# Kernel tuning notes

Hardware: AMD Instinct MI355X
Metric: run time of the kernel (lower is better)

Reference implementation:

```python
import jax, jax.numpy as jnp
import numpy as np

B, T, C, H = 4, 2048, 1024, 16
D = C // H  # head dim = 64
ROPE_BASE = 10000.0


def _rope_cache(seq_len, dim, dtype=jnp.float32):
    # torchtune-style interleaved RoPE cache
    inv_freq = 1.0 / (ROPE_BASE ** (jnp.arange(0, dim, 2, dtype=jnp.float32) / dim))
    t = jnp.arange(seq_len, dtype=jnp.float32)
    freqs = jnp.outer(t, inv_freq)  # [T, D/2]
    return jnp.cos(freqs).astype(dtype), jnp.sin(freqs).astype(dtype)


def _apply_rope(x, cos, sin):
    # x: [B, H, T, D]; rotate interleaved pairs along last dim
    x1 = x[..., 0::2]
    x2 = x[..., 1::2]
    # broadcast cos/sin [T, D/2] -> [1, 1, T, D/2]
    o1 = x1 * cos - x2 * sin
    o2 = x2 * cos + x1 * sin
    out = jnp.stack([o1, o2], axis=-1).reshape(x.shape)
    return out


def setup_inputs() -> dict:
    key = jax.random.key(0)
    k1, k2, k3 = jax.random.split(key, 3)
    x = jax.random.normal(k1, (B, T, C), dtype=jnp.float32)
    W_in = jax.random.normal(k2, (C, 3 * C), dtype=jnp.float32) * (1.0 / np.sqrt(C))
    b_in = jnp.zeros((3 * C,), dtype=jnp.float32)
    W_out = jax.random.normal(k3, (C, C), dtype=jnp.float32) * (1.0 / np.sqrt(C))
    b_out = jnp.zeros((C,), dtype=jnp.float32)
    return {"x": x, "W_in": W_in, "b_in": b_in, "W_out": W_out, "b_out": b_out}


def reference(x, W_in, b_in, W_out, b_out):
    Bx, Tx, Cx = x.shape
    qkv = x @ W_in + b_in                      # [B, T, 3C]
    q, k, v = jnp.split(qkv, 3, axis=-1)
    # [B, T, C] -> [B, H, T, D]
    def to_heads(t):
        return t.reshape(Bx, Tx, H, D).transpose(0, 2, 1, 3)
    q, k, v = to_heads(q), to_heads(k), to_heads(v)

    cos, sin = _rope_cache(Tx, D, dtype=x.dtype)
    q = _apply_rope(q, cos, sin)
    k = _apply_rope(k, cos, sin)

    scale = 1.0 / np.sqrt(D)
    att = jnp.einsum('bhqd,bhkd->bhqk', q, k) * scale   # [B, H, T, T]
    causal = jnp.tril(jnp.ones((Tx, Tx), dtype=bool))
    att = jnp.where(causal[None, None, :, :], att, jnp.float32(-jnp.inf).astype(att.dtype))
    att = jax.nn.softmax(att, axis=-1)
    # dropout = 0.0 (eval mode): identity
    y = jnp.einsum('bhqk,bhkd->bhqd', att, v)           # [B, H, T, D]
    y = y.transpose(0, 2, 1, 3).reshape(Bx, Tx, Cx)     # [B, T, C]
    return y @ W_out + b_out
```

## Files before the change

### kernel.cpp

```cpp
#include <hip/hip_runtime.h>

#define B_ 4
#define T_ 2048
#define C_ 1024
#define H_ 16
#define D_ 64
#define M_ (B_*T_)
#define N3_ (3*C_)
#define NQT_ 16

typedef unsigned short u16;
typedef short bf16x8 __attribute__((ext_vector_type(8)));
typedef short bf16x4 __attribute__((ext_vector_type(4)));
typedef unsigned short u16x8 __attribute__((ext_vector_type(8)));
typedef unsigned int u32x4 __attribute__((ext_vector_type(4)));
typedef float f32x4 __attribute__((ext_vector_type(4)));
typedef float f32x16 __attribute__((ext_vector_type(16)));

#define QSCALE 0.18033688f
#define DEFER_THR 11.0f

__device__ __forceinline__ u16 f2bf(float f) {
  unsigned u = __float_as_uint(f);
  u += 0x7fffu + ((u >> 16) & 1u);
  return (u16)(u >> 16);
}

__device__ __forceinline__ unsigned cvt_pk_bf16(float lo, float hi) {
  unsigned r;
  asm("v_cvt_pk_bf16_f32 %0, %1, %2" : "=v"(r) : "v"(lo), "v"(hi));
  return r;
}

__device__ __forceinline__ void gload16(const void* g, void* l) {
  __builtin_amdgcn_global_load_lds((const __attribute__((address_space(1))) void*)g,
                                   (__attribute__((address_space(3))) void*)l, 16, 0, 0);
}

__device__ __forceinline__ int epi_key(int ml) { return (ml ^ (ml >> 3)) & 7; }

__global__ __launch_bounds__(256) void k_prep(const float* __restrict__ x,
                                              u16* __restrict__ xbf,
                                              const float* __restrict__ W_in,
                                              u16* __restrict__ WtIn,
                                              const float* __restrict__ W_out,
                                              u16* __restrict__ WtOut,
                                              float* __restrict__ ct,
                                              float* __restrict__ st) {
  __shared__ float tile[64][65];
  const int bx = blockIdx.x, tid = threadIdx.x;
  if (bx < 4096) {
    int i = bx * 256 + tid;
    f32x4 a = *(const f32x4*)(x + (size_t)i * 8);
    f32x4 b = *(const f32x4*)(x + (size_t)i * 8 + 4);
    u16x8 o;
    #pragma unroll
    for (int j = 0; j < 4; ++j) { o[j] = f2bf(a[j]); o[4 + j] = f2bf(b[j]); }
    *(u16x8*)(xbf + (size_t)i * 8) = o;
  } else if (bx < 5120) {
    const float* W; u16* Wt; int K = C_, N, b;
    if (bx < 4864) { W = W_in; Wt = WtIn; N = N3_; b = bx - 4096; }
    else           { W = W_out; Wt = WtOut; N = C_; b = bx - 4864; }
    int ntiles = N / 64;
    int n0 = (b % ntiles) * 64, k0 = (b / ntiles) * 64;
    int c = tid & 63, r0 = tid >> 6;
    #pragma unroll
    for (int i = 0; i < 16; ++i) {
      int r = i * 4 + r0;
      tile[r][c] = W[(size_t)(k0 + r) * N + n0 + c];
    }
    __syncthreads();
    #pragma unroll
    for (int i = 0; i < 16; ++i) {
      int r = i * 4 + r0;
      Wt[(size_t)(n0 + r) * K + k0 + c] = f2bf(tile[c][r]);
    }
  } else {
    int idx = (bx - 5120) * 256 + tid;
    int t = idx >> 5, i = idx & 31;
    double inv = exp(-(2.0 * (double)i / 64.0) * log(10000.0));
    double a = (double)t * inv;
    ct[idx] = (float)cos(a);
    st[idx] = (float)sin(a);
  }
}

__global__ __launch_bounds__(512) void k_gemm1(const u16* __restrict__ A,
                                               const u16* __restrict__ Bt,
                                               const float* __restrict__ bias,
                                               u16* __restrict__ Qb, u16* __restrict__ Kb,
                                               u16* __restrict__ Vt,
                                               const float* __restrict__ ctab,
                                               const float* __restrict__ stab) {
  __shared__ u16 lds[128 * 64 + 256 * 64];
  u16* sA = lds;
  u16* sB = lds + 128 * 64;
  const int tid = threadIdx.x, lane = tid & 63, w = tid >> 6;
  const int g = lane >> 4, r = lane & 15;
  const int wm = w >> 2, wn = w & 3;
  const int Kd = C_;
  const int lin = blockIdx.y * gridDim.x + blockIdx.x;
  const int tM = ((lin & 7) * 8 + ((lin >> 3) & 7)) * 128;
  const int tN = (lin >> 6) * 256;

  f32x4 acc[4][4];
  #pragma unroll
  for (int i = 0; i < 4; ++i)
    #pragma unroll
    for (int j = 0; j < 4; ++j) acc[i][j] = (f32x4){0.f, 0.f, 0.f, 0.f};

  for (int k0 = 0; k0 < Kd; k0 += 64) {
    #pragma unroll
    for (int i = 0; i < 2; ++i) {
      int c = i * 512 + tid, row = c >> 3, slot = (c & 7) ^ (row & 7);
      gload16(A + (size_t)(tM + row) * Kd + k0 + slot * 8, sA + (i * 512 + w * 64) * 8);
    }
    #pragma unroll
    for (int i = 0; i < 4; ++i) {
      int c = i * 512 + tid, row = c >> 3, slot = (c & 7) ^ (row & 7);
      gload16(Bt + (size_t)(tN + row) * Kd + k0 + slot * 8, sB + (i * 512 + w * 64) * 8);
    }
    __syncthreads();
    bf16x8 af[4][2], bfr[4][2];
    #pragma unroll
    for (int mt = 0; mt < 4; ++mt)
      #pragma unroll
      for (int kk = 0; kk < 2; ++kk) {
        int row = wm * 64 + mt * 16 + r;
        af[mt][kk] = *(const bf16x8*)(sA + ((row * 64 + kk * 32 + g * 8) ^ ((row & 7) << 3)));
      }
    #pragma unroll
    for (int nt = 0; nt < 4; ++nt)
      #pragma unroll
      for (int kk = 0; kk < 2; ++kk) {
        int row = wn * 64 + nt * 16 + r;
        bfr[nt][kk] = *(const bf16x8*)(sB + ((row * 64 + kk * 32 + g * 8) ^ ((row & 7) << 3)));
      }
    __builtin_amdgcn_s_setprio(1);
    #pragma unroll
    for (int mt = 0; mt < 4; ++mt)
      #pragma unroll
      for (int nt = 0; nt < 4; ++nt)
        #pragma unroll
        for (int kk = 0; kk < 2; ++kk)
          acc[mt][nt] = __builtin_amdgcn_mfma_f32_16x16x32_bf16(af[mt][kk], bfr[nt][kk],
                                                                acc[mt][nt], 0, 0, 0);
    __builtin_amdgcn_s_setprio(0);
    __syncthreads();
  }

  const int secb = tN >> 10;
  u16* tile = lds;
  const int bb = tM >> 11;
  #pragma unroll
  for (int hN = 0; hN < 2; ++hN) {
    if ((wn >> 1) == hN) {
      #pragma unroll
      for (int mt = 0; mt < 4; ++mt)
        #pragma unroll
        for (int nt = 0; nt < 4; ++nt) {
          int nl = (wn & 1) * 64 + nt * 16 + r;
          int n = tN + hN * 128 + nl;
          float bv = bias[n];
          int dd = n & 63;
          #pragma unroll
          for (int reg = 0; reg < 4; ++reg) {
            int ml = wm * 64 + mt * 16 + g * 4 + reg;
            int tt = (tM + ml) & (T_ - 1);
            float v = acc[mt][nt][reg] + bv;
            if (secb < 2) {
              float pv = __shfl_xor(v, 1);
              int pi = tt * 32 + (dd >> 1);
              float c = ctab[pi], sn = stab[pi];
              v = (dd & 1) ? (v * c + pv * sn) : (v * c - pv * sn);
              if (secb == 0) v *= QSCALE;
            }
            tile[ml * 128 + ((((nl >> 3) ^ epi_key(ml)) << 3) | (nl & 7))] = f2bf(v);
          }
        }
    }
    __syncthreads();
    if (secb < 2) {
      u16* dst = secb == 0 ? Qb : Kb;
      #pragma unroll
      for (int i = 0; i < 4; ++i) {
        int idx = i * 512 + tid;
        int row = idx >> 4, cc = idx & 15;
        u16x8 val = *(const u16x8*)(tile + row * 128 + ((cc ^ epi_key(row)) << 3));
        int n = tN + hN * 128 + cc * 8;
        int m = tM + row;
        int hh = (n & 1023) >> 6, dd = n & 63;
        int tt = m & (T_ - 1);
        *(u16x8*)(dst + ((size_t)(bb * H_ + hh) * T_ + tt) * D_ + dd) = val;
      }
    } else {
      const int tt0 = tM & (T_ - 1);
      #pragma unroll
      for (int i = 0; i < 4; ++i) {
        int idx = i * 512 + tid;
        int nl = idx >> 4, tg = idx & 15;
        u16x8 val;
        #pragma unroll
        for (int j = 0; j < 8; ++j) {
          int ml = tg * 8 + j;
          val[j] = tile[ml * 128 + ((((nl >> 3) ^ epi_key(ml)) << 3) | (nl & 7))];
        }
        int n = tN + hN * 128 + nl;
        int hh = (n & 1023) >> 6, dd = n & 63;
        *(u16x8*)(Vt + ((size_t)(bb * H_ + hh) * D_ + dd) * T_ + tt0 + tg * 8) = val;
      }
    }
    __syncthreads();
  }
}

__global__ __launch_bounds__(256) void k_gemm2(const u16* __restrict__ A,
                                               const u16* __restrict__ Bt,
                                               const float* __restrict__ bias,
                                               float* __restrict__ Cout,
                                               int Nd, int Kd) {
  __shared__ u16 sA[128 * 128];
  __shared__ u16 sB[128 * 128];
  const int tid = threadIdx.x, lane = tid & 63, w = tid >> 6;
  const int g = lane >> 4, r = lane & 15;
  const int wm = w >> 1, wn = w & 1;
  const int lin = blockIdx.y * gridDim.x + blockIdx.x;
  const int tM = ((lin & 7) * 8 + ((lin >> 3) & 7)) * 128;
  const int tN = (lin >> 6) * 128;

  f32x4 acc[4][4];
  #pragma unroll
  for (int i = 0; i < 4; ++i)
    #pragma unroll
    for (int j = 0; j < 4; ++j) acc[i][j] = (f32x4){0.f, 0.f, 0.f, 0.f};

  for (int k0 = 0; k0 < Kd; k0 += 128) {
    #pragma unroll
    for (int i = 0; i < 8; ++i) {
      int c = i * 256 + tid, row = c >> 4, slot = (c & 15) ^ (row & 15);
      gload16(A + (size_t)(tM + row) * Kd + k0 + slot * 8, sA + (i * 256 + w * 64) * 8);
    }
    #pragma unroll
    for (int i = 0; i < 8; ++i) {
      int c = i * 256 + tid, row = c >> 4, slot = (c & 15) ^ (row & 15);
      gload16(Bt + (size_t)(tN + row) * Kd + k0 + slot * 8, sB + (i * 256 + w * 64) * 8);
    }
    __syncthreads();
    #pragma unroll
    for (int kk = 0; kk < 4; ++kk) {
      bf16x8 af[4], bfr[4];
      #pragma unroll
      for (int mt = 0; mt < 4; ++mt) {
        int row = wm * 64 + mt * 16 + r;
        af[mt] = *(const bf16x8*)(sA + row * 128 + (((kk * 4 + g) ^ (row & 15)) * 8));
      }
      #pragma unroll
      for (int nt = 0; nt < 4; ++nt) {
        int row = wn * 64 + nt * 16 + r;
        bfr[nt] = *(const bf16x8*)(sB + row * 128 + (((kk * 4 + g) ^ (row & 15)) * 8));
      }
      __builtin_amdgcn_s_setprio(1);
      #pragma unroll
      for (int mt = 0; mt < 4; ++mt)
        #pragma unroll
        for (int nt = 0; nt < 4; ++nt)
          acc[mt][nt] = __builtin_amdgcn_mfma_f32_16x16x32_bf16(af[mt], bfr[nt],
                                                                acc[mt][nt], 0, 0, 0);
      __builtin_amdgcn_s_setprio(0);
    }
    __syncthreads();
  }

  #pragma unroll
  for (int mt = 0; mt < 4; ++mt)
    #pragma unroll
    for (int nt = 0; nt < 4; ++nt) {
      int n = tN + wn * 64 + nt * 16 + r;
      float bv = bias[n];
      #pragma unroll
      for (int reg = 0; reg < 4; ++reg) {
        int m = tM + wm * 64 + mt * 16 + g * 4 + reg;
        Cout[(size_t)m * Nd + n] = acc[mt][nt][reg] + bv;
      }
    }
}

__global__ __launch_bounds__(256) void k_attn(const u16* __restrict__ Qb,
                                              const u16* __restrict__ Kb,
                                              const u16* __restrict__ Vt,
                                              u16* __restrict__ Y) {
  __shared__ u16 sK[2][64 * 64];
  __shared__ u16 sV[2][64 * 64];
  const int tid = threadIdx.x, w = tid >> 6;
  const int lane = tid & 63, col = lane & 31, hi = lane >> 5;
  const int pair = blockIdx.x;
  const int h = blockIdx.y, b = blockIdx.z;
  const size_t bhK = ((size_t)b * H_ + h) * T_;
  const size_t bhV = ((size_t)b * H_ + h) * D_;

  const int qtA = pair, qtB = (NQT_ - 1) - pair;
  const int ntA = 2 * qtA + 2;
  const int total = 2 * (NQT_ - 1) + 4;

  auto STAGE = [&](int buf, int kt) {
    #pragma unroll
    for (int i = 0; i < 2; ++i) {
      int c = i * 256 + tid, row = c >> 3, slot = (c & 7) ^ (row & 7);
      gload16(Kb + (bhK + kt * 64 + row) * D_ + slot * 8, &sK[buf][(i * 256 + w * 64) * 8]);
    }
    #pragma unroll
    for (int i = 0; i < 2; ++i) {
      int c = i * 256 + tid, row = c >> 3, slot = (c & 7) ^ (row & 7);
      gload16(Vt + (bhV + row) * T_ + kt * 64 + slot * 8, &sV[buf][(i * 256 + w * 64) * 8]);
    }
  };

  int qw = qtA * 128 + w * 32;
  int tq = qw + col;
  bf16x8 qf[4];
  #pragma unroll
  for (int c = 0; c < 4; ++c)
    qf[c] = *(const bf16x8*)(Qb + (bhK + tq) * D_ + c * 16 + hi * 8);

  float m_run = -3e38f, l_run = 0.f;
  f32x16 o0, o1;
  #pragma unroll
  for (int i = 0; i < 16; ++i) { o0[i] = 0.f; o1[i] = 0.f; }

  auto FINAL = [&]() {
    float lr = l_run + __shfl_xor(l_run, 32);
    float rl = 1.0f / lr;
    u16* yrow = Y + ((size_t)b * T_ + tq) * C_ + h * 64;
    #pragma unroll
    for (int dt = 0; dt < 2; ++dt)
      #pragma unroll
      for (int j = 0; j < 8; ++j) {
        float a0 = (dt ? o1[2 * j] : o0[2 * j]) * rl;
        float a1 = (dt ? o1[2 * j + 1] : o0[2 * j + 1]) * rl;
        int d = dt * 32 + 8 * (j >> 1) + 4 * hi + 2 * (j & 1);
        *(unsigned*)(yrow + d) = cvt_pk_bf16(a0, a1);
      }
  };

  STAGE(0, 0);
  __syncthreads();

  for (int it = 0; it < total; ++it) {
    const int cur = it & 1;
    if (it + 1 < total) {
      int nit = it + 1;
      STAGE(cur ^ 1, nit < ntA ? nit : nit - ntA);
    }
    const int ktl = it < ntA ? it : it - ntA;
    const int kb = ktl * 64;
    if (kb <= qw + 31) {
      const bool act1 = (kb + 32 <= qw + 31);
      f32x16 s0, s1;
      #pragma unroll
      for (int i = 0; i < 16; ++i) { s0[i] = 0.f; s1[i] = 0.f; }

      __builtin_amdgcn_s_setprio(1);
      #pragma unroll
      for (int c = 0; c < 4; ++c) {
        int row = col;
        bf16x8 kf = *(const bf16x8*)(&sK[cur][(row * 64 + c * 16 + hi * 8) ^ ((row & 7) << 3)]);
        s0 = __builtin_amdgcn_mfma_f32_32x32x16_bf16(kf, qf[c], s0, 0, 0, 0);
      }
      if (act1) {
        #pragma unroll
        for (int c = 0; c < 4; ++c) {
          int row = 32 + col;
          bf16x8 kf = *(const bf16x8*)(&sK[cur][(row * 64 + c * 16 + hi * 8) ^ ((row & 7) << 3)]);
          s1 = __builtin_amdgcn_mfma_f32_32x32x16_bf16(kf, qf[c], s1, 0, 0, 0);
        }
      }
      __builtin_amdgcn_s_setprio(0);

      if (kb + 31 > qw) {
        #pragma unroll
        for (int reg = 0; reg < 16; ++reg) {
          int key = kb + (reg & 3) + 8 * (reg >> 2) + 4 * hi;
          if (key > tq) s0[reg] = -3e38f;
        }
      }
      if (act1 && kb + 63 > qw) {
        #pragma unroll
        for (int reg = 0; reg < 16; ++reg) {
          int key = kb + 32 + (reg & 3) + 8 * (reg >> 2) + 4 * hi;
          if (key > tq) s1[reg] = -3e38f;
        }
      }

      float pm = s0[0];
      #pragma unroll
      for (int reg = 1; reg < 16; ++reg) pm = fmaxf(pm, s0[reg]);
      if (act1) {
        #pragma unroll
        for (int reg = 0; reg < 16; ++reg) pm = fmaxf(pm, s1[reg]);
      }
      if (__any(pm > m_run + DEFER_THR)) {
        float tm = fmaxf(pm, __shfl_xor(pm, 32));
        float mn = fmaxf(m_run, tm);
        float f = __builtin_amdgcn_exp2f(m_run - mn);
        m_run = mn;
        #pragma unroll
        for (int i = 0; i < 16; ++i) { o0[i] *= f; o1[i] *= f; }
        l_run *= f;
      }

      #pragma unroll
      for (int reg = 0; reg < 16; ++reg) {
        s0[reg] = __builtin_amdgcn_exp2f(s0[reg] - m_run);
        l_run += s0[reg];
      }
      if (act1) {
        #pragma unroll
        for (int reg = 0; reg < 16; ++reg) {
          s1[reg] = __builtin_amdgcn_exp2f(s1[reg] - m_run);
          l_run += s1[reg];
        }
      }

      __builtin_amdgcn_s_setprio(1);
      #pragma unroll
      for (int st = 0; st < 2; ++st) {
        if (st == 1 && !act1) break;
        #pragma unroll
        for (int u = 0; u < 2; ++u) {
          u32x4 pw;
          #pragma unroll
          for (int j = 0; j < 4; ++j) {
            int jr = (4 * u + j) * 2;
            pw[j] = st ? cvt_pk_bf16(s1[jr], s1[jr + 1])
                       : cvt_pk_bf16(s0[jr], s0[jr + 1]);
          }
          bf16x8 pf = __builtin_bit_cast(bf16x8, pw);
          const int keybase = st * 32 + u * 16;
          #pragma unroll
          for (int dt = 0; dt < 2; ++dt) {
            int row = dt * 32 + col;
            int e0 = (row * 64 + keybase + 4 * hi) ^ ((row & 7) << 3);
            int e1 = (row * 64 + keybase + 8 + 4 * hi) ^ ((row & 7) << 3);
            bf16x4 vlo = *(const bf16x4*)(&sV[cur][e0]);
            bf16x4 vhi = *(const bf16x4*)(&sV[cur][e1]);
            bf16x8 vf;
            vf[0] = vlo[0]; vf[1] = vlo[1]; vf[2] = vlo[2]; vf[3] = vlo[3];
            vf[4] = vhi[0]; vf[5] = vhi[1]; vf[6] = vhi[2]; vf[7] = vhi[3];
            if (dt == 0) o0 = __builtin_amdgcn_mfma_f32_32x32x16_bf16(vf, pf, o0, 0, 0, 0);
            else         o1 = __builtin_amdgcn_mfma_f32_32x32x16_bf16(vf, pf, o1, 0, 0, 0);
          }
        }
      }
      __builtin_amdgcn_s_setprio(0);
    }
    __syncthreads();

    if (it == ntA - 1) {
      FINAL();
      qw = qtB * 128 + w * 32;
      tq = qw + col;
      #pragma unroll
      for (int c = 0; c < 4; ++c)
        qf[c] = *(const bf16x8*)(Qb + (bhK + tq) * D_ + c * 16 + hi * 8);
      m_run = -3e38f; l_run = 0.f;
      #pragma unroll
      for (int i = 0; i < 16; ++i) { o0[i] = 0.f; o1[i] = 0.f; }
    }
  }
  FINAL();
}

extern "C" void kernel_launch(void* const* d_in, const int* in_sizes, int n_in,
                              void* d_out, int out_size, void* d_ws, size_t ws_size,
                              hipStream_t stream) {
  const float* x     = (const float*)d_in[0];
  const float* W_in  = (const float*)d_in[1];
  const float* b_in  = (const float*)d_in[2];
  const float* W_out = (const float*)d_in[3];
  const float* b_out = (const float*)d_in[4];
  float* out = (float*)d_out;

  const size_t NE = (size_t)B_ * H_ * T_ * D_;
  u16* Qb    = (u16*)d_ws;
  u16* Kb    = Qb + NE;
  u16* Vt    = Kb + NE;
  u16* xbf   = Vt + NE;
  u16* WtIn  = xbf + (size_t)M_ * C_;
  u16* WtOut = WtIn + (size_t)N3_ * C_;
  float* ctab = (float*)(WtOut + (size_t)C_ * C_);
  float* stab = ctab + T_ * 32;
  u16* ybf = xbf;

  size_t needed = (size_t)((char*)(stab + T_ * 32) - (char*)d_ws);
  if (ws_size < needed) return;

  k_prep<<<5376, 256, 0, stream>>>(x, xbf, W_in, WtIn, W_out, WtOut, ctab, stab);

  k_gemm1<<<dim3(N3_ / 256, M_ / 128), 512, 0, stream>>>(
      xbf, WtIn, b_in, Qb, Kb, Vt, ctab, stab);

  k_attn<<<dim3(NQT_ / 2, H_, B_), 256, 0, stream>>>(Qb, Kb, Vt, ybf);

  k_gemm2<<<dim3(C_ / 128, M_ / 128), 256, 0, stream>>>(
      ybf, WtOut, b_out, out, C_, C_);
}
```

Measured before the change: 223.6 us.

## Restructure QKV GEMM to 256x128 tiles with 4 waves, two M accumulators

```diff
diff --git a/kernel.cpp b/kernel.cpp
--- a/kernel.cpp
+++ b/kernel.cpp
@@ -85,133 +85,160 @@
   }
 }
 
-__global__ __launch_bounds__(512) void k_gemm1(const u16* __restrict__ A,
+__global__ __launch_bounds__(256) void k_gemm1(const u16* __restrict__ A,
                                                const u16* __restrict__ Bt,
                                                const float* __restrict__ bias,
                                                u16* __restrict__ Qb, u16* __restrict__ Kb,
                                                u16* __restrict__ Vt,
                                                const float* __restrict__ ctab,
                                                const float* __restrict__ stab) {
-  __shared__ u16 lds[128 * 64 + 256 * 64];
-  u16* sA = lds;
-  u16* sB = lds + 128 * 64;
+  __shared__ u16 lds[3 * 128 * 64];
+  u16* sA0 = lds;
+  u16* sA1 = lds + 8192;
+  u16* sB  = lds + 16384;
   const int tid = threadIdx.x, lane = tid & 63, w = tid >> 6;
   const int g = lane >> 4, r = lane & 15;
-  const int wm = w >> 2, wn = w & 3;
+  const int wm = w >> 1, wn = w & 1;
   const int Kd = C_;
   const int lin = blockIdx.y * gridDim.x + blockIdx.x;
-  const int tM = ((lin & 7) * 8 + ((lin >> 3) & 7)) * 128;
-  const int tN = (lin >> 6) * 256;
-
-  f32x4 acc[4][4];
+  const int tM = ((lin & 7) * 4 + ((lin >> 3) & 3)) * 256;
+  const int tN = (lin >> 5) * 128;
+
+  f32x4 acc0[4][4], acc1[4][4];
   #pragma unroll
   for (int i = 0; i < 4; ++i)
     #pragma unroll
-    for (int j = 0; j < 4; ++j) acc[i][j] = (f32x4){0.f, 0.f, 0.f, 0.f};
+    for (int j = 0; j < 4; ++j) {
+      acc0[i][j] = (f32x4){0.f, 0.f, 0.f, 0.f};
+      acc1[i][j] = (f32x4){0.f, 0.f, 0.f, 0.f};
+    }
 
   for (int k0 = 0; k0 < Kd; k0 += 64) {
     #pragma unroll
-    for (int i = 0; i < 2; ++i) {
-      int c = i * 512 + tid, row = c >> 3, slot = (c & 7) ^ (row & 7);
-      gload16(A + (size_t)(tM + row) * Kd + k0 + slot * 8, sA + (i * 512 + w * 64) * 8);
-    }
-    #pragma unroll
     for (int i = 0; i < 4; ++i) {
-      int c = i * 512 + tid, row = c >> 3, slot = (c & 7) ^ (row & 7);
-      gload16(Bt + (size_t)(tN + row) * Kd + k0 + slot * 8, sB + (i * 512 + w * 64) * 8);
-    }
-    __syncthreads();
-    bf16x8 af[4][2], bfr[4][2];
+      int c = i * 256 + tid, row = c >> 3, slot = (c & 7) ^ (row & 7);
+      gload16(A + (size_t)(tM + row) * Kd + k0 + slot * 8, sA0 + (i * 256 + w * 64) * 8);
+    }
+    #pragma unroll
+    for (int i = 0; i < 4; ++i) {
+      int c = i * 256 + tid, row = c >> 3, slot = (c & 7) ^ (row & 7);
+      gload16(A + (size_t)(tM + 128 + row) * Kd + k0 + slot * 8, sA1 + (i * 256 + w * 64) * 8);
+    }
+    #pragma unroll
+    for (int i = 0; i < 4; ++i) {
+      int c = i * 256 + tid, row = c >> 3, slot = (c & 7) ^ (row & 7);
+      gload16(Bt + (size_t)(tN + row) * Kd + k0 + slot * 8, sB + (i * 256 + w * 64) * 8);
+    }
+    __syncthreads();
+    #pragma unroll
+    for (int kk = 0; kk < 2; ++kk) {
+      bf16x8 bfr[4];
+      #pragma unroll
+      for (int nt = 0; nt < 4; ++nt) {
+        int row = wn * 64 + nt * 16 + r;
+        bfr[nt] = *(const bf16x8*)(sB + ((row * 64 + kk * 32 + g * 8) ^ ((row & 7) << 3)));
+      }
+      {
+        bf16x8 af[4];
+        #pragma unroll
+        for (int mt = 0; mt < 4; ++mt) {
+          int row = wm * 64 + mt * 16 + r;
+          af[mt] = *(const bf16x8*)(sA0 + ((row * 64 + kk * 32 + g * 8) ^ ((row & 7) << 3)));
+        }
+        __builtin_amdgcn_s_setprio(1);
+        #pragma unroll
+        for (int mt = 0; mt < 4; ++mt)
+          #pragma unroll
+          for (int nt = 0; nt < 4; ++nt)
+            acc0[mt][nt] = __builtin_amdgcn_mfma_f32_16x16x32_bf16(af[mt], bfr[nt],
+                                                                   acc0[mt][nt], 0, 0, 0);
+        __builtin_amdgcn_s_setprio(0);
+      }
+      {
+        bf16x8 af[4];
+        #pragma unroll
+        for (int mt = 0; mt < 4; ++mt) {
+          int row = wm * 64 + mt * 16 + r;
+          af[mt] = *(const bf16x8*)(sA1 + ((row * 64 + kk * 32 + g * 8) ^ ((row & 7) << 3)));
+        }
+        __builtin_amdgcn_s_setprio(1);
+        #pragma unroll
+        for (int mt = 0; mt < 4; ++mt)
+          #pragma unroll
+          for (int nt = 0; nt < 4; ++nt)
+            acc1[mt][nt] = __builtin_amdgcn_mfma_f32_16x16x32_bf16(af[mt], bfr[nt],
+                                                                   acc1[mt][nt], 0, 0, 0);
+        __builtin_amdgcn_s_setprio(0);
+      }
+    }
+    __syncthreads();
+  }
+
+  const int secb = tN >> 10;
+  const int bb = tM >> 11;
+  u16* tile = lds;
+
+  auto EPI = [&](f32x4 (&acc)[4][4], int mOff) {
     #pragma unroll
     for (int mt = 0; mt < 4; ++mt)
       #pragma unroll
-      for (int kk = 0; kk < 2; ++kk) {
-        int row = wm * 64 + mt * 16 + r;
-        af[mt][kk] = *(const bf16x8*)(sA + ((row * 64 + kk * 32 + g * 8) ^ ((row & 7) << 3)));
-      }
-    #pragma unroll
-    for (int nt = 0; nt < 4; ++nt)
-      #pragma unroll
-      for (int kk = 0; kk < 2; ++kk) {
-        int row = wn * 64 + nt * 16 + r;
-        bfr[nt][kk] = *(const bf16x8*)(sB + ((row * 64 + kk * 32 + g * 8) ^ ((row & 7) << 3)));
-      }
-    __builtin_amdgcn_s_setprio(1);
-    #pragma unroll
-    for (int mt = 0; mt < 4; ++mt)
-      #pragma unroll
-      for (int nt = 0; nt < 4; ++nt)
-        #pragma unroll
-        for (int kk = 0; kk < 2; ++kk)
-          acc[mt][nt] = __builtin_amdgcn_mfma_f32_16x16x32_bf16(af[mt][kk], bfr[nt][kk],
-                                                                acc[mt][nt], 0, 0, 0);
-    __builtin_amdgcn_s_setprio(0);
-    __syncthreads();
-  }
-
-  const int secb = tN >> 10;
-  u16* tile = lds;
-  const int bb = tM >> 11;
-  #pragma unroll
-  for (int hN = 0; hN < 2; ++hN) {
-    if ((wn >> 1) == hN) {
-      #pragma unroll
-      for (int mt = 0; mt < 4; ++mt)
-        #pragma unroll
-        for (int nt = 0; nt < 4; ++nt) {
-          int nl = (wn & 1) * 64 + nt * 16 + r;
-          int n = tN + hN * 128 + nl;
-          float bv = bias[n];
-          int dd = n & 63;
-          #pragma unroll
-          for (int reg = 0; reg < 4; ++reg) {
-            int ml = wm * 64 + mt * 16 + g * 4 + reg;
-            int tt = (tM + ml) & (T_ - 1);
-            float v = acc[mt][nt][reg] + bv;
-            if (secb < 2) {
-              float pv = __shfl_xor(v, 1);
-              int pi = tt * 32 + (dd >> 1);
-              float c = ctab[pi], sn = stab[pi];
-              v = (dd & 1) ? (v * c + pv * sn) : (v * c - pv * sn);
-              if (secb == 0) v *= QSCALE;
-            }
-            tile[ml * 128 + ((((nl >> 3) ^ epi_key(ml)) << 3) | (nl & 7))] = f2bf(v);
+      for (int nt = 0; nt < 4; ++nt) {
+        int nl = wn * 64 + nt * 16 + r;
+        int n = tN + nl;
+        float bv = bias[n];
+        int dd = n & 63;
+        #pragma unroll
+        for (int reg = 0; reg < 4; ++reg) {
+          int ml = wm * 64 + mt * 16 + g * 4 + reg;
+          int tt = (tM + mOff + ml) & (T_ - 1);
+          float v = acc[mt][nt][reg] + bv;
+          if (secb < 2) {
+            float pv = __shfl_xor(v, 1);
+            int pi = tt * 32 + (dd >> 1);
+            float c = ctab[pi], sn = stab[pi];
+            v = (dd & 1) ? (v * c + pv * sn) : (v * c - pv * sn);
+            if (secb == 0) v *= QSCALE;
           }
-        }
-    }
+          tile[ml * 128 + ((((nl >> 3) ^ epi_key(ml)) << 3) | (nl & 7))] = f2bf(v);
+        }
+      }
     __syncthreads();
     if (secb < 2) {
       u16* dst = secb == 0 ? Qb : Kb;
       #pragma unroll
-      for (int i = 0; i < 4; ++i) {
-        int idx = i * 512 + tid;
-        int row = idx >> 4, cc = idx & 15;
+      for (int i = 0; i < 8; ++i) {
+        int row = w * 32 + (i & 3) * 8 + (lane >> 3);
+        int cc = (i >> 2) * 8 + (lane & 7);
         u16x8 val = *(const u16x8*)(tile + row * 128 + ((cc ^ epi_key(row)) << 3));
-        int n = tN + hN * 128 + cc * 8;
-        int m = tM + row;
+        int n = tN + cc * 8;
+        int m = tM + mOff + row;
         int hh = (n & 1023) >> 6, dd = n & 63;
         int tt = m & (T_ - 1);
         *(u16x8*)(dst + ((size_t)(bb * H_ + hh) * T_ + tt) * D_ + dd) = val;
       }
     } else {
-      const int tt0 = tM & (T_ - 1);
-      #pragma unroll
-      for (int i = 0; i < 4; ++i) {
-        int idx = i * 512 + tid;
-        int nl = idx >> 4, tg = idx & 15;
+      const int tt0 = (tM + mOff) & (T_ - 1);
+      #pragma unroll
+      for (int v = 0; v < 8; ++v) {
+        int idx = v * 256 + tid;
+        int nl = idx >> 4;
+        int tg = idx & 15;
         u16x8 val;
         #pragma unroll
         for (int j = 0; j < 8; ++j) {
           int ml = tg * 8 + j;
           val[j] = tile[ml * 128 + ((((nl >> 3) ^ epi_key(ml)) << 3) | (nl & 7))];
         }
-        int n = tN + hN * 128 + nl;
+        int n = tN + nl;
         int hh = (n & 1023) >> 6, dd = n & 63;
         *(u16x8*)(Vt + ((size_t)(bb * H_ + hh) * D_ + dd) * T_ + tt0 + tg * 8) = val;
       }
     }
     __syncthreads();
-  }
+  };
+
+  EPI(acc0, 0);
+  EPI(acc1, 128);
 }
 
 __global__ __launch_bounds__(256) void k_gemm2(const u16* __restrict__ A,
@@ -496,7 +523,7 @@
 
   k_prep<<<5376, 256, 0, stream>>>(x, xbf, W_in, WtIn, W_out, WtOut, ctab, stab);
 
-  k_gemm1<<<dim3(N3_ / 256, M_ / 128), 512, 0, stream>>>(
+  k_gemm1<<<dim3(N3_ / 128, M_ / 256), 256, 0, stream>>>(
       xbf, WtIn, b_in, Qb, Kb, Vt, ctab, stab);
 
   k_attn<<<dim3(NQT_ / 2, H_, B_), 256, 0, stream>>>(Qb, Kb, Vt, ybf);
```

Measured after the change: 237.9 us. +6.4%, slower.
